# Kernel tuning notes

Measured on AMD Instinct MI355X. Metric: run time of the kernel, lower is better.

The kernel has to match this reference:

```python
import jax, jax.numpy as jnp
import numpy as np

B, C = 32768, 1000

def setup_inputs() -> dict:
    key = jax.random.key(0)
    k1, k2 = jax.random.split(key)
    pred = jax.random.normal(k1, (B, C), dtype=jnp.float32)
    target = jax.random.randint(k2, (B,), 0, C, dtype=jnp.int64)
    return {"pred": pred, "target": target}

def reference(pred, target):
    b, c = pred.shape
    # histogram of labels: replaces the per-class Python loop
    class_freq = jnp.zeros((c,), dtype=pred.dtype).at[target].add(1.0)
    # exp(pred) * freq, then log-normalize over classes (balanced softmax)
    scaled = jnp.exp(pred) * class_freq  # [B, C]
    log_norm = jnp.log(jnp.sum(scaled, axis=1, keepdims=True))  # [B, 1]
    logits = jnp.log(scaled) - log_norm  # [B, C]
    # one-hot multiply + sum == gather logit at target class
    picked = jnp.take_along_axis(logits, target[:, None], axis=1)  # [B, 1]
    return -jnp.sum(picked) / b
```

## Files before the change

kernel.cpp:

```cpp
#include <hip/hip_runtime.h>

#define B_ROWS 32768
#define C_COLS 1000
#define NF4 250
#define HIST_BLOCKS 16
#define MAIN_BLOCKS 2048

__global__ __launch_bounds__(256) void bsl_hist(const int* __restrict__ target,
                                                float* __restrict__ freq_part) {
    __shared__ unsigned int lh[C_COLS];
    const int tid = threadIdx.x;
    for (int i = tid; i < C_COLS; i += 256) lh[i] = 0u;
    __syncthreads();
    const int4* t4 = reinterpret_cast<const int4*>(target + blockIdx.x * 2048);
    #pragma unroll
    for (int k = 0; k < 2; ++k) {
        int4 v = t4[tid + k * 256];
        atomicAdd(&lh[v.x], 1u);
        atomicAdd(&lh[v.y], 1u);
        atomicAdd(&lh[v.z], 1u);
        atomicAdd(&lh[v.w], 1u);
    }
    __syncthreads();
    float* dst = freq_part + blockIdx.x * C_COLS;
    for (int i = tid; i < C_COLS; i += 256) dst[i] = (float)lh[i];
}

__global__ __launch_bounds__(256) void bsl_main(const float* __restrict__ pred,
                                                const int* __restrict__ target,
                                                const float* __restrict__ freq_part,
                                                float* __restrict__ partials) {
    __shared__ float sfreq[C_COLS];
    __shared__ float swave[4];
    const int tid = threadIdx.x;
    const int lane = tid & 63;
    const int wib = tid >> 6;

    for (int i = tid; i < C_COLS; i += 256) {
        float s = 0.0f;
        #pragma unroll
        for (int b = 0; b < HIST_BLOCKS; ++b) s += freq_part[b * C_COLS + i];
        sfreq[i] = s;
    }
    __syncthreads();
    const float4* sf4 = reinterpret_cast<const float4*>(sfreq);

    const int base = (blockIdx.x * 4 + wib) * 4;
    float local = 0.0f;

    #pragma unroll
    for (int p = 0; p < 2; ++p) {
        const int r0 = base + p * 2;
        const int r1 = r0 + 1;
        const int t0 = target[r0], t1 = target[r1];
        const float4* p0 = reinterpret_cast<const float4*>(pred + (size_t)r0 * C_COLS);
        const float4* p1 = reinterpret_cast<const float4*>(pred + (size_t)r1 * C_COLS);
        const int t4i0 = t0 >> 2, tm0 = t0 & 3;
        const int t4i1 = t1 >> 2, tm1 = t1 & 3;

        float4 v0[4], v1[4];
        #pragma unroll
        for (int k = 0; k < 4; ++k) {
            const int j = k * 64 + lane;
            if (j < NF4) v0[k] = p0[j];
        }
        #pragma unroll
        for (int k = 0; k < 4; ++k) {
            const int j = k * 64 + lane;
            if (j < NF4) v1[k] = p1[j];
        }

        float s0 = 0.0f, s1 = 0.0f, pt0 = 0.0f, pt1 = 0.0f;
        #pragma unroll
        for (int k = 0; k < 4; ++k) {
            const int j = k * 64 + lane;
            if (j < NF4) {
                const float4 f = sf4[j];
                const float4 a = v0[k];
                const float4 b = v1[k];
                s0 += __expf(a.x) * f.x + __expf(a.y) * f.y
                    + __expf(a.z) * f.z + __expf(a.w) * f.w;
                s1 += __expf(b.x) * f.x + __expf(b.y) * f.y
                    + __expf(b.z) * f.z + __expf(b.w) * f.w;
                if (j == t4i0)
                    pt0 = (tm0 & 1) ? ((tm0 & 2) ? a.w : a.y)
                                    : ((tm0 & 2) ? a.z : a.x);
                if (j == t4i1)
                    pt1 = (tm1 & 1) ? ((tm1 & 2) ? b.w : b.y)
                                    : ((tm1 & 2) ? b.z : b.x);
            }
        }
        #pragma unroll
        for (int off = 32; off > 0; off >>= 1) {
            s0 += __shfl_xor(s0, off, 64);
            s1 += __shfl_xor(s1, off, 64);
        }
        const float ptb0 = __shfl(pt0, t4i0 & 63, 64);
        const float ptb1 = __shfl(pt1, t4i1 & 63, 64);
        local += logf(s0) - ptb0 - logf(sfreq[t0]);
        local += logf(s1) - ptb1 - logf(sfreq[t1]);
    }

    if (lane == 0) swave[wib] = local;
    __syncthreads();
    if (tid == 0)
        partials[blockIdx.x] = swave[0] + swave[1] + swave[2] + swave[3];
}

__global__ __launch_bounds__(256) void bsl_finalize(const float* __restrict__ partials,
                                                    float* __restrict__ out) {
    const int tid = threadIdx.x;
    float s = 0.0f;
    for (int i = tid; i < MAIN_BLOCKS; i += 256) s += partials[i];
    #pragma unroll
    for (int off = 32; off > 0; off >>= 1) s += __shfl_xor(s, off, 64);
    __shared__ float sw[4];
    if ((tid & 63) == 0) sw[tid >> 6] = s;
    __syncthreads();
    if (tid == 0) out[0] = (sw[0] + sw[1] + sw[2] + sw[3]) / (float)B_ROWS;
}

extern "C" void kernel_launch(void* const* d_in, const int* in_sizes, int n_in,
                              void* d_out, int out_size, void* d_ws, size_t ws_size,
                              hipStream_t stream) {
    const float* pred = (const float*)d_in[0];
    const int* target = (const int*)d_in[1];

    float* freq_part = (float*)d_ws;
    float* partials  = freq_part + HIST_BLOCKS * C_COLS;

    bsl_hist<<<HIST_BLOCKS, 256, 0, stream>>>(target, freq_part);
    bsl_main<<<MAIN_BLOCKS, 256, 0, stream>>>(pred, target, freq_part, partials);
    bsl_finalize<<<1, 256, 0, stream>>>(partials, (float*)d_out);
}
```

Baseline: 39.84 us.

## Merge histogram with global atomics and halve rows per main-kernel wave

```diff
diff --git a/kernel.cpp b/kernel.cpp
--- a/kernel.cpp
+++ b/kernel.cpp
@@ -3,11 +3,10 @@
 #define B_ROWS 32768
 #define C_COLS 1000
 #define NF4 250
-#define HIST_BLOCKS 16
-#define MAIN_BLOCKS 2048
+#define MAIN_BLOCKS 4096
 
 __global__ __launch_bounds__(256) void bsl_hist(const int* __restrict__ target,
-                                                float* __restrict__ freq_part) {
+                                                float* __restrict__ freq) {
     __shared__ unsigned int lh[C_COLS];
     const int tid = threadIdx.x;
     for (int i = tid; i < C_COLS; i += 256) lh[i] = 0u;
@@ -22,13 +21,15 @@
         atomicAdd(&lh[v.w], 1u);
     }
     __syncthreads();
-    float* dst = freq_part + blockIdx.x * C_COLS;
-    for (int i = tid; i < C_COLS; i += 256) dst[i] = (float)lh[i];
+    for (int i = tid; i < C_COLS; i += 256) {
+        unsigned int c = lh[i];
+        if (c) atomicAdd(&freq[i], (float)c);
+    }
 }
 
 __global__ __launch_bounds__(256) void bsl_main(const float* __restrict__ pred,
                                                 const int* __restrict__ target,
-                                                const float* __restrict__ freq_part,
+                                                const float* __restrict__ freq,
                                                 float* __restrict__ partials) {
     __shared__ float sfreq[C_COLS];
     __shared__ float swave[4];
@@ -36,70 +37,59 @@
     const int lane = tid & 63;
     const int wib = tid >> 6;
 
-    for (int i = tid; i < C_COLS; i += 256) {
-        float s = 0.0f;
-        #pragma unroll
-        for (int b = 0; b < HIST_BLOCKS; ++b) s += freq_part[b * C_COLS + i];
-        sfreq[i] = s;
-    }
+    for (int i = tid; i < C_COLS; i += 256) sfreq[i] = freq[i];
     __syncthreads();
     const float4* sf4 = reinterpret_cast<const float4*>(sfreq);
 
-    const int base = (blockIdx.x * 4 + wib) * 4;
-    float local = 0.0f;
+    const int r0 = (blockIdx.x * 4 + wib) * 2;
+    const int r1 = r0 + 1;
+    const int t0 = target[r0], t1 = target[r1];
+    const float4* p0 = reinterpret_cast<const float4*>(pred + (size_t)r0 * C_COLS);
+    const float4* p1 = reinterpret_cast<const float4*>(pred + (size_t)r1 * C_COLS);
+    const int t4i0 = t0 >> 2, tm0 = t0 & 3;
+    const int t4i1 = t1 >> 2, tm1 = t1 & 3;
 
+    float4 v0[4], v1[4];
     #pragma unroll
-    for (int p = 0; p < 2; ++p) {
-        const int r0 = base + p * 2;
-        const int r1 = r0 + 1;
-        const int t0 = target[r0], t1 = target[r1];
-        const float4* p0 = reinterpret_cast<const float4*>(pred + (size_t)r0 * C_COLS);
-        const float4* p1 = reinterpret_cast<const float4*>(pred + (size_t)r1 * C_COLS);
-        const int t4i0 = t0 >> 2, tm0 = t0 & 3;
-        const int t4i1 = t1 >> 2, tm1 = t1 & 3;
+    for (int k = 0; k < 4; ++k) {
+        const int j = k * 64 + lane;
+        if (j < NF4) v0[k] = p0[j];
+    }
+    #pragma unroll
+    for (int k = 0; k < 4; ++k) {
+        const int j = k * 64 + lane;
+        if (j < NF4) v1[k] = p1[j];
+    }
 
-        float4 v0[4], v1[4];
-        #pragma unroll
-        for (int k = 0; k < 4; ++k) {
-            const int j = k * 64 + lane;
-            if (j < NF4) v0[k] = p0[j];
+    float s0 = 0.0f, s1 = 0.0f, pt0 = 0.0f, pt1 = 0.0f;
+    #pragma unroll
+    for (int k = 0; k < 4; ++k) {
+        const int j = k * 64 + lane;
+        if (j < NF4) {
+            const float4 f = sf4[j];
+            const float4 a = v0[k];
+            const float4 b = v1[k];
+            s0 += __expf(a.x) * f.x + __expf(a.y) * f.y
+                + __expf(a.z) * f.z + __expf(a.w) * f.w;
+            s1 += __expf(b.x) * f.x + __expf(b.y) * f.y
+                + __expf(b.z) * f.z + __expf(b.w) * f.w;
+            if (j == t4i0)
+                pt0 = (tm0 & 1) ? ((tm0 & 2) ? a.w : a.y)
+                                : ((tm0 & 2) ? a.z : a.x);
+            if (j == t4i1)
+                pt1 = (tm1 & 1) ? ((tm1 & 2) ? b.w : b.y)
+                                : ((tm1 & 2) ? b.z : b.x);
         }
-        #pragma unroll
-        for (int k = 0; k < 4; ++k) {
-            const int j = k * 64 + lane;
-            if (j < NF4) v1[k] = p1[j];
-        }
-
-        float s0 = 0.0f, s1 = 0.0f, pt0 = 0.0f, pt1 = 0.0f;
-        #pragma unroll
-        for (int k = 0; k < 4; ++k) {
-            const int j = k * 64 + lane;
-            if (j < NF4) {
-                const float4 f = sf4[j];
-                const float4 a = v0[k];
-                const float4 b = v1[k];
-                s0 += __expf(a.x) * f.x + __expf(a.y) * f.y
-                    + __expf(a.z) * f.z + __expf(a.w) * f.w;
-                s1 += __expf(b.x) * f.x + __expf(b.y) * f.y
-                    + __expf(b.z) * f.z + __expf(b.w) * f.w;
-                if (j == t4i0)
-                    pt0 = (tm0 & 1) ? ((tm0 & 2) ? a.w : a.y)
-                                    : ((tm0 & 2) ? a.z : a.x);
-                if (j == t4i1)
-                    pt1 = (tm1 & 1) ? ((tm1 & 2) ? b.w : b.y)
-                                    : ((tm1 & 2) ? b.z : b.x);
-            }
-        }
-        #pragma unroll
-        for (int off = 32; off > 0; off >>= 1) {
-            s0 += __shfl_xor(s0, off, 64);
-            s1 += __shfl_xor(s1, off, 64);
-        }
-        const float ptb0 = __shfl(pt0, t4i0 & 63, 64);
-        const float ptb1 = __shfl(pt1, t4i1 & 63, 64);
-        local += logf(s0) - ptb0 - logf(sfreq[t0]);
-        local += logf(s1) - ptb1 - logf(sfreq[t1]);
     }
+    #pragma unroll
+    for (int off = 32; off > 0; off >>= 1) {
+        s0 += __shfl_xor(s0, off, 64);
+        s1 += __shfl_xor(s1, off, 64);
+    }
+    const float ptb0 = __shfl(pt0, t4i0 & 63, 64);
+    const float ptb1 = __shfl(pt1, t4i1 & 63, 64);
+    float local = logf(s0) - ptb0 - logf(sfreq[t0])
+                + logf(s1) - ptb1 - logf(sfreq[t1]);
 
     if (lane == 0) swave[wib] = local;
     __syncthreads();
@@ -126,10 +116,12 @@
     const float* pred = (const float*)d_in[0];
     const int* target = (const int*)d_in[1];
 
-    float* freq_part = (float*)d_ws;
-    float* partials  = freq_part + HIST_BLOCKS * C_COLS;
+    float* freq     = (float*)d_ws;
+    float* partials = freq + 1024;
 
-    bsl_hist<<<HIST_BLOCKS, 256, 0, stream>>>(target, freq_part);
-    bsl_main<<<MAIN_BLOCKS, 256, 0, stream>>>(pred, target, freq_part, partials);
+    hipMemsetAsync(freq, 0, 1024 * sizeof(float), stream);
+
+    bsl_hist<<<16, 256, 0, stream>>>(target, freq);
+    bsl_main<<<MAIN_BLOCKS, 256, 0, stream>>>(pred, target, freq, partials);
     bsl_finalize<<<1, 256, 0, stream>>>(partials, (float*)d_out);
 }
```

New measurement: 38.49 us. -3.4%, faster.
